# Optimization experiments

Measured on AMD Instinct MI355X. Metric: run time of the kernel, lower is better.

## Reference

```python
import jax, jax.numpy as jnp
import numpy as np

N = 30000        # nodes
E = 600000       # edges
R = 32           # relations
NB = 30          # num_bases
D = 128          # entity_dim == hidden_dim == output_dim
H = 8            # heads, head dim C = D // H = 16
NUM_ENT = 100000
NGRAPH = 16      # graphs in batch
L = 2            # num_rgcn_layers == num_transformer_layers
EPS = 1e-5


def _ln(x, g, b):
    mu = x.mean(-1, keepdims=True)
    var = ((x - mu) ** 2).mean(-1, keepdims=True)
    return (x - mu) * jax.lax.rsqrt(var + EPS) * g + b


def setup_inputs() -> dict:
    key = jax.random.key(0)
    ks = iter(jax.random.split(key, 48))

    def nrm(shape, s=0.05):
        return jax.random.normal(next(ks), shape, jnp.float32) * s

    inp = {}
    inp["node_ids"] = jax.random.randint(next(ks), (N,), 0, NUM_ENT)
    inp["edge_index"] = jax.random.randint(next(ks), (2, E), 0, N)
    inp["edge_type"] = jax.random.randint(next(ks), (E,), 0, R)
    inp["batch"] = jnp.sort(jax.random.randint(next(ks), (N,), 0, NGRAPH))
    inp["entity_emb"] = nrm((NUM_ENT, D)).at[0].set(0.0)  # padding_idx=0
    inp["rel_emb"] = nrm((R, D)).at[0].set(0.0)           # padding_idx=0
    inp["rgcn_comp"] = nrm((L, R, NB))
    inp["rgcn_bases"] = nrm((L, NB, D, D))
    inp["rgcn_root"] = nrm((L, D, D))
    inp["rgcn_bias"] = jnp.zeros((L, D), jnp.float32)
    inp["rgcn_ln_g"] = jnp.ones((L, D), jnp.float32)
    inp["rgcn_ln_b"] = jnp.zeros((L, D), jnp.float32)
    inp["tr_wq"] = nrm((L, D, D)); inp["tr_bq"] = jnp.zeros((L, D), jnp.float32)
    inp["tr_wk"] = nrm((L, D, D)); inp["tr_bk"] = jnp.zeros((L, D), jnp.float32)
    inp["tr_wv"] = nrm((L, D, D)); inp["tr_bv"] = jnp.zeros((L, D), jnp.float32)
    inp["tr_we"] = nrm((L, D, D))                          # lin_edge (bias=False in PyG)
    inp["tr_wskip"] = nrm((L, D, D)); inp["tr_bskip"] = jnp.zeros((L, D), jnp.float32)
    inp["tr_ln_g"] = jnp.ones((L, D), jnp.float32)
    inp["tr_ln_b"] = jnp.zeros((L, D), jnp.float32)
    return inp


def reference(node_ids, edge_index, edge_type, batch, entity_emb, rel_emb,
              rgcn_comp, rgcn_bases, rgcn_root, rgcn_bias, rgcn_ln_g, rgcn_ln_b,
              tr_wq, tr_bq, tr_wk, tr_bk, tr_wv, tr_bv, tr_we, tr_wskip, tr_bskip,
              tr_ln_g, tr_ln_b):
    src, tgt = edge_index[0], edge_index[1]
    C = D // H
    x = entity_emb[node_ids]            # [N, D]
    edge_attr = rel_emb[edge_type]      # [E, D]

    # ---- RGCN layers: basis decomposition, mean aggregation per (target, relation) ----
    seg = tgt * R + edge_type
    cnt = jax.ops.segment_sum(jnp.ones((E,), jnp.float32), seg, num_segments=N * R)
    inv = jnp.where(cnt > 0, 1.0 / jnp.maximum(cnt, 1.0), 0.0)   # [N*R]
    for l in range(L):
        agg = jax.ops.segment_sum(x[src], seg, num_segments=N * R)   # [N*R, D]
        agg = (agg * inv[:, None]).reshape(N, R, D)
        w = jnp.einsum('rb,bio->rio', rgcn_comp[l], rgcn_bases[l])   # [R, D, D]
        x = jnp.einsum('nri,rio->no', agg, w) + x @ rgcn_root[l] + rgcn_bias[l]
        x = jax.nn.relu(_ln(x, rgcn_ln_g[l], rgcn_ln_b[l]))          # dropout = identity (eval)

    # ---- TransformerConv layers: edge-conditioned multi-head attention ----
    for l in range(L):
        q = (x @ tr_wq[l] + tr_bq[l]).reshape(N, H, C)
        k = (x @ tr_wk[l] + tr_bk[l]).reshape(N, H, C)
        v = (x @ tr_wv[l] + tr_bv[l]).reshape(N, H, C)
        e = (edge_attr @ tr_we[l]).reshape(E, H, C)
        kj = k[src] + e                                              # [E, H, C]
        vj = v[src] + e
        alpha = jnp.einsum('ehc,ehc->eh', q[tgt], kj) / np.float32(np.sqrt(C))
        m = jax.ops.segment_max(alpha, tgt, num_segments=N)          # [N, H]
        a = jnp.exp(alpha - m[tgt])
        denom = jax.ops.segment_sum(a, tgt, num_segments=N)
        a = a / jnp.maximum(denom[tgt], 1e-16)                       # softmax per target node
        out = jax.ops.segment_sum((vj * a[:, :, None]).reshape(E, D), tgt, num_segments=N)
        out = out + x @ tr_wskip[l] + tr_bskip[l]                    # root/skip connection
        out = jax.nn.relu(_ln(out, tr_ln_g[l], tr_ln_b[l]))          # dropout = identity (eval)
        x = x + out                                                  # dims match -> residual

    cnt_g = jax.ops.segment_sum(jnp.ones((N,), jnp.float32), batch, num_segments=NGRAPH)
    graph_emb = jax.ops.segment_sum(x, batch, num_segments=NGRAPH) / jnp.maximum(cnt_g, 1.0)[:, None]
    return x, graph_emb
```

## Files before the change

kernel.cpp:

```cpp
#include <hip/hip_runtime.h>

#define NN 30000
#define NE 600000
#define RR 32
#define NBASE 30
#define NG 16

typedef long long i64;
typedef unsigned short ushort;
typedef short bf16x8 __attribute__((ext_vector_type(8)));
typedef float f32x4 __attribute__((ext_vector_type(4)));

__device__ __forceinline__ ushort f2bf(float f){
  unsigned u = __float_as_uint(f);
  u += 0x7fffu + ((u >> 16) & 1u);
  return (ushort)(u >> 16);
}
__device__ __forceinline__ float bf2f(ushort u){
  return __uint_as_float(((unsigned)u) << 16);
}
__device__ __forceinline__ unsigned pk2(float a, float b){
  return (unsigned)f2bf(a) | ((unsigned)f2bf(b) << 16);
}

__global__ void k_gather(const float* __restrict__ emb, const int* __restrict__ ids,
                         float* __restrict__ x, ushort* __restrict__ xb){
  int t = blockIdx.x*256 + threadIdx.x;
  if (t >= NN*32) return;
  int n = t >> 5, c = t & 31;
  float4 v = ((const float4*)emb)[(i64)ids[n]*32 + c];
  ((float4*)x)[(i64)n*32 + c] = v;
  *(uint2*)&xb[(i64)n*128 + c*4] = make_uint2(pk2(v.x, v.y), pk2(v.z, v.w));
}

__global__ __launch_bounds__(256) void k_stats(const int* __restrict__ etgt,
    const int* __restrict__ ety, float* __restrict__ cnt,
    int* __restrict__ hist, int* __restrict__ hist2){
  __shared__ int lh[RR];
  if (threadIdx.x < RR) lh[threadIdx.x] = 0;
  __syncthreads();
  int e0 = blockIdx.x*2048 + threadIdx.x;
  #pragma unroll
  for (int i = 0; i < 8; i++){
    int e = e0 + i*256;
    if (e < NE){
      int tgt = etgt[e], r = ety[e];
      atomicAdd(&lh[r], 1);
      atomicAdd(&hist2[tgt], 1);
      atomicAdd(&cnt[(i64)tgt*RR + r], 1.0f);
    }
  }
  __syncthreads();
  if (threadIdx.x < RR){
    int v = lh[threadIdx.x];
    if (v) atomicAdd(&hist[threadIdx.x], v);
  }
}

__global__ __launch_bounds__(1024) void k_scan2(const int* __restrict__ hist2,
    int* __restrict__ rowptr, int* __restrict__ cursor2,
    const int* __restrict__ hist, int* __restrict__ base,
    int* __restrict__ cursor, int* __restrict__ pb, int* __restrict__ pb64){
  int t = threadIdx.x;
  if (t == 0){
    int s = 0, p = 0, p64 = 0;
    for (int r = 0; r < RR; r++){
      base[r] = s; cursor[r] = s; pb[r] = p; pb64[r] = p64;
      s += hist[r]; p += (hist[r] + 127) >> 7; p64 += (hist[r] + 63) >> 6;
    }
    base[RR] = s; pb[RR] = p; pb64[RR] = p64;
  }
  __shared__ int s[1024];
  int bse = t*30;
  int loc[30];
  int sum = 0;
  #pragma unroll
  for (int i = 0; i < 30; i++){
    int v = (bse+i < NN) ? hist2[bse+i] : 0;
    loc[i] = sum; sum += v;
  }
  s[t] = sum; __syncthreads();
  for (int off = 1; off < 1024; off <<= 1){
    int v = (t >= off) ? s[t-off] : 0;
    __syncthreads();
    s[t] += v;
    __syncthreads();
  }
  int excl = (t > 0) ? s[t-1] : 0;
  #pragma unroll
  for (int i = 0; i < 30; i++){
    int idx = bse + i;
    if (idx <= NN){
      rowptr[idx] = excl + loc[i];
      if (idx < NN) cursor2[idx] = excl + loc[i];
    }
  }
}

__global__ void k_scatter2(const int* __restrict__ etgt, const int* __restrict__ esrc,
                           const int* __restrict__ ety, int* __restrict__ cursor2,
                           int2* __restrict__ se2, int* __restrict__ pos2){
  int e = blockIdx.x*256 + threadIdx.x;
  if (e >= NE) return;
  int q = atomicAdd(&cursor2[etgt[e]], 1);
  se2[q] = make_int2(esrc[e], ety[e]);
  pos2[e] = q;
  if (e < 8) se2[NE + e] = make_int2(0, 0);
}

__global__ __launch_bounds__(256) void k_scatter_blk(const int* __restrict__ ety,
    const int* __restrict__ esrc, const int* __restrict__ etgt,
    const int* __restrict__ pos2, const float* __restrict__ cnt,
    int* __restrict__ cursor, int* __restrict__ eord,
    int* __restrict__ sg_src, int* __restrict__ sg_p2, float* __restrict__ sg_inv){
  __shared__ int lh[RR];
  __shared__ int lb[RR];
  if (threadIdx.x < RR) lh[threadIdx.x] = 0;
  __syncthreads();
  int e0 = blockIdx.x*2048 + threadIdx.x;
  #pragma unroll
  for (int i = 0; i < 8; i++){
    int e = e0 + i*256;
    if (e < NE) atomicAdd(&lh[ety[e]], 1);
  }
  __syncthreads();
  if (threadIdx.x < RR){
    int c = lh[threadIdx.x];
    lb[threadIdx.x] = c ? atomicAdd(&cursor[threadIdx.x], c) : 0;
  }
  __syncthreads();
  if (threadIdx.x < RR) lh[threadIdx.x] = 0;
  __syncthreads();
  #pragma unroll
  for (int i = 0; i < 8; i++){
    int e = e0 + i*256;
    if (e < NE){
      int r = ety[e];
      int loc = atomicAdd(&lh[r], 1);
      int slot = lb[r] + loc;
      eord[slot]   = e;
      sg_src[slot] = esrc[e];
      sg_p2[slot]  = pos2[e];
      sg_inv[slot] = 1.0f / cnt[(i64)etgt[e]*RR + r];
    }
  }
}

__global__ void k_basis(const float* __restrict__ comp, const float* __restrict__ bases,
                        float* __restrict__ wT, ushort* __restrict__ wTb){
  int t = blockIdx.x*256 + threadIdx.x;
  int r = t >> 14, rem = t & 16383, c = rem >> 7, kk = rem & 127;
  float acc = 0.f;
  for (int b = 0; b < NBASE; b++)
    acc += comp[r*NBASE + b] * bases[(i64)b*16384 + kk*128 + c];
  wT[t] = acc;
  wTb[t] = f2bf(acc);
}

__global__ void k_tw(const float* __restrict__ root, const float* __restrict__ wq,
                     const float* __restrict__ wk, const float* __restrict__ wv,
                     const float* __restrict__ wsk, ushort* __restrict__ out){
  int z = blockIdx.y;
  const float* srcs[5] = {root, wq, wk, wv, wsk};
  const float* S = srcs[z >> 1] + (i64)(z & 1)*16384;
  int idx = blockIdx.x*256 + threadIdx.x;
  int c = idx >> 7, kk = idx & 127;
  out[(i64)z*16384 + idx] = f2bf(S[kk*128 + c]);
}


__global__ __launch_bounds__(256, 4) void k_mm_mfma(const ushort* __restrict__ xb,
    const ushort* __restrict__ wTb, const float* __restrict__ bias,
    float* __restrict__ Y, int nrows){
  __shared__ ushort Xs[16384];
  int t = threadIdx.x;
  int row0 = blockIdx.x * 128;
  for (int i = t; i < 2048; i += 256){
    int row = i >> 4, c = i & 15;
    int gr = min(row0 + row, nrows - 1);
    *(uint4*)((char*)Xs + row*256 + ((c*16) ^ ((row&7)<<4))) =
        *(const uint4*)((const char*)(xb + (i64)gr*128) + c*16);
  }
  __syncthreads();
  int w = t >> 6, l = t & 63;
  int wm = w >> 1, wn = w & 1;
  int lrow = l & 15, lg = l >> 4;
  int swz = (lrow & 7) << 4;
  const char* pX = (const char*)Xs + (wm*64 + lrow)*256;
  const char* pW = (const char*)wTb + (wn*64 + lrow)*256 + 16*lg;
  f32x4 acc[4][4] = {};
  #pragma unroll
  for (int ks = 0; ks < 4; ks++){
    int kb = (16*lg + 64*ks) ^ swz;
    bf16x8 a[4], bx[4];
    #pragma unroll
    for (int ns = 0; ns < 4; ns++) a[ns]  = *(const bf16x8*)(pW + ns*4096 + 64*ks);
    #pragma unroll
    for (int ms = 0; ms < 4; ms++) bx[ms] = *(const bf16x8*)(pX + ms*4096 + kb);
    #pragma unroll
    for (int ms = 0; ms < 4; ms++)
      #pragma unroll
      for (int ns = 0; ns < 4; ns++)
        acc[ms][ns] = __builtin_amdgcn_mfma_f32_16x16x32_bf16(a[ns], bx[ms], acc[ms][ns], 0, 0, 0);
  }
  #pragma unroll
  for (int ms = 0; ms < 4; ms++){
    int m = row0 + wm*64 + ms*16 + lrow;
    if (m >= nrows) continue;
    #pragma unroll
    for (int ns = 0; ns < 4; ns++){
      int n0 = wn*64 + ns*16 + 4*lg;
      float4 bv = *(const float4*)&bias[n0];
      f32x4 v = acc[ms][ns];
      *(float4*)&Y[(i64)m*128 + n0] =
          make_float4(v[0]+bv.x, v[1]+bv.y, v[2]+bv.z, v[3]+bv.w);
    }
  }
}

__global__ __launch_bounds__(256, 4) void k_mm4(const ushort* __restrict__ xb,
    const ushort* __restrict__ wTb, int layer,
    const float* __restrict__ biq, const float* __restrict__ bik,
    const float* __restrict__ biv, const float* __restrict__ bisk,
    ushort* __restrict__ qo, ushort* __restrict__ ko, ushort* __restrict__ vo,
    float* __restrict__ z, int nrows){
  __shared__ ushort Xs[16384];
  int t = threadIdx.x;
  int row0 = blockIdx.x * 128;
  for (int i = t; i < 2048; i += 256){
    int row = i >> 4, c = i & 15;
    int gr = min(row0 + row, nrows - 1);
    *(uint4*)((char*)Xs + row*256 + ((c*16) ^ ((row&7)<<4))) =
        *(const uint4*)((const char*)(xb + (i64)gr*128) + c*16);
  }
  __syncthreads();
  int w = t >> 6, l = t & 63;
  int wm = w >> 1, wn = w & 1;
  int lrow = l & 15, lg = l >> 4;
  int swz = (lrow & 7) << 4;
  const char* pX = (const char*)Xs + (wm*64 + lrow)*256;
  const float* biases[4] = {biq, bik, biv, bisk};
  ushort* outs[3] = {qo, ko, vo};
  #pragma unroll 1
  for (int arr = 0; arr < 4; arr++){
    const char* pW = (const char*)(wTb + (i64)(2 + 2*arr + layer)*16384)
                     + (wn*64 + lrow)*256 + 16*lg;
    f32x4 acc[4][4] = {};
    #pragma unroll
    for (int ks = 0; ks < 4; ks++){
      int kb = (16*lg + 64*ks) ^ swz;
      bf16x8 a[4], bx[4];
      #pragma unroll
      for (int ns = 0; ns < 4; ns++) a[ns]  = *(const bf16x8*)(pW + ns*4096 + 64*ks);
      #pragma unroll
      for (int ms = 0; ms < 4; ms++) bx[ms] = *(const bf16x8*)(pX + ms*4096 + kb);
      #pragma unroll
      for (int ms = 0; ms < 4; ms++)
        #pragma unroll
        for (int ns = 0; ns < 4; ns++)
          acc[ms][ns] = __builtin_amdgcn_mfma_f32_16x16x32_bf16(a[ns], bx[ms], acc[ms][ns], 0, 0, 0);
    }
    const float* bias = biases[arr];
    #pragma unroll
    for (int ms = 0; ms < 4; ms++){
      int m = row0 + wm*64 + ms*16 + lrow;
      if (m >= nrows) continue;
      #pragma unroll
      for (int ns = 0; ns < 4; ns++){
        int n0 = wn*64 + ns*16 + 4*lg;
        float4 bv = *(const float4*)&bias[n0];
        f32x4 v = acc[ms][ns];
        if (arr < 3){
          *(uint2*)&outs[arr][(i64)m*128 + n0] =
              make_uint2(pk2(v[0]+bv.x, v[1]+bv.y), pk2(v[2]+bv.z, v[3]+bv.w));
        } else {
          *(float4*)&z[(i64)m*128 + n0] =
              make_float4(v[0]+bv.x, v[1]+bv.y, v[2]+bv.z, v[3]+bv.w);
        }
      }
    }
  }
}

__global__ __launch_bounds__(256, 4) void k_edge_mfma(
    const int* __restrict__ sg_src, const int* __restrict__ sg_p2,
    const float* __restrict__ sg_inv, const int* __restrict__ hist,
    const int* __restrict__ base, const int* __restrict__ pb,
    const ushort* __restrict__ xb, const ushort* __restrict__ wb,
    ushort* __restrict__ y){
  __shared__ ushort Xs[16384];
  __shared__ int s_src[128];
  __shared__ int s_p2[128];
  __shared__ float s_inv[128];
  int b = blockIdx.x;
  int r = -1;
  #pragma unroll 1
  for (int i = 0; i < RR; i++){
    if (b >= pb[i] && b < pb[i+1]) { r = i; break; }
  }
  if (r < 0) return;
  int chunk = b - pb[r];
  int rowbase = base[r] + chunk*128;
  int nvalid = min(128, hist[r] - chunk*128);
  int t = threadIdx.x;
  if (t < 128){
    bool valid = t < nvalid;
    int slot = rowbase + (valid ? t : 0);
    s_src[t] = sg_src[slot];
    s_p2[t]  = valid ? sg_p2[slot] : NE;
    s_inv[t] = valid ? sg_inv[slot] : 0.0f;
  }
  __syncthreads();
  for (int i = t; i < 2048; i += 256){
    int row = i >> 4, c = i & 15;
    *(uint4*)((char*)Xs + row*256 + ((c*16) ^ ((row&7)<<4))) =
        *(const uint4*)((const char*)(xb + (i64)s_src[row]*128) + c*16);
  }
  __syncthreads();
  int w = t >> 6, l = t & 63;
  int wm = w >> 1, wn = w & 1;
  int lrow = l & 15, lg = l >> 4;
  int swz = (lrow & 7) << 4;
  const char* pX = (const char*)Xs + (wm*64 + lrow)*256;
  const char* pW = (const char*)(wb + (i64)r*16384) + (wn*64 + lrow)*256 + 16*lg;
  f32x4 acc[4][4] = {};
  #pragma unroll
  for (int ks = 0; ks < 4; ks++){
    int kb = (16*lg + 64*ks) ^ swz;
    bf16x8 a[4], bx[4];
    #pragma unroll
    for (int ns = 0; ns < 4; ns++) a[ns]  = *(const bf16x8*)(pW + ns*4096 + 64*ks);
    #pragma unroll
    for (int ms = 0; ms < 4; ms++) bx[ms] = *(const bf16x8*)(pX + ms*4096 + kb);
    #pragma unroll
    for (int ms = 0; ms < 4; ms++)
      #pragma unroll
      for (int ns = 0; ns < 4; ns++)
        acc[ms][ns] = __builtin_amdgcn_mfma_f32_16x16x32_bf16(a[ns], bx[ms], acc[ms][ns], 0, 0, 0);
  }
  __syncthreads();
  #pragma unroll
  for (int ms = 0; ms < 4; ms++){
    int m = wm*64 + ms*16 + lrow;
    float sc = s_inv[m];
    int msk = (m & 7) << 4;
    #pragma unroll
    for (int ns = 0; ns < 4; ns++){
      int n0 = wn*64 + ns*16 + 4*lg;
      f32x4 v = acc[ms][ns];
      *(uint2*)((char*)Xs + m*256 + ((n0*2) ^ msk)) =
          make_uint2(pk2(v[0]*sc, v[1]*sc), pk2(v[2]*sc, v[3]*sc));
    }
  }
  __syncthreads();
  for (int i = t; i < 2048; i += 256){
    int row = i >> 4, c = i & 15;
    uint4 v = *(const uint4*)((const char*)Xs + row*256 + ((c*16) ^ ((row&7)<<4)));
    *(uint4*)&y[(i64)s_p2[row]*128 + c*8] = v;
  }
}

__global__ __launch_bounds__(256) void k_edge_atomic(const int* __restrict__ esrc,
    const int* __restrict__ etgt, const int* __restrict__ eord,
    const int* __restrict__ hist, const int* __restrict__ base,
    const int* __restrict__ pb, const float* __restrict__ cnt,
    const float* __restrict__ x, const float* __restrict__ wT,
    float* __restrict__ z){
  __shared__ float Xs[64][132];
  __shared__ int s_src[64];
  __shared__ int s_tgt[64];
  __shared__ float s_inv[64];
  int b = blockIdx.x;
  int r = -1;
  #pragma unroll 1
  for (int i = 0; i < RR; i++){
    if (b >= pb[i] && b < pb[i+1]) { r = i; break; }
  }
  if (r < 0) return;
  int chunk = b - pb[r];
  int rowbase = base[r] + chunk*64;
  int cnt_r = hist[r];
  if (threadIdx.x < 64){
    int i = threadIdx.x;
    bool valid = (chunk*64 + i) < cnt_r;
    int eid = valid ? eord[rowbase + i] : 0;
    int sv = valid ? esrc[eid] : 0;
    int tv = valid ? etgt[eid] : 0;
    s_src[i] = sv; s_tgt[i] = tv;
    s_inv[i] = valid ? (1.0f / cnt[(i64)tv*RR + r]) : 0.0f;
  }
  __syncthreads();
  for (int idx = threadIdx.x; idx < 64*32; idx += 256){
    int rr = idx >> 5, c4 = idx & 31;
    *(float4*)&Xs[rr][c4*4] = ((const float4*)x)[(i64)s_src[rr]*32 + c4];
  }
  __syncthreads();
  const float* W = wT + (i64)r*16384;
  int m = threadIdx.x & 15, cg = threadIdx.x >> 4;
  float acc[4][8] = {};
  #pragma unroll 2
  for (int k4 = 0; k4 < 128; k4 += 4){
    float4 xv[4], wv[8];
    #pragma unroll
    for (int i = 0; i < 4; i++) xv[i] = *(float4*)&Xs[m + 16*i][k4];
    #pragma unroll
    for (int j = 0; j < 8; j++) wv[j] = *(const float4*)&W[(i64)(cg + 16*j)*128 + k4];
    #pragma unroll
    for (int i = 0; i < 4; i++)
      #pragma unroll
      for (int j = 0; j < 8; j++)
        acc[i][j] += xv[i].x*wv[j].x + xv[i].y*wv[j].y + xv[i].z*wv[j].z + xv[i].w*wv[j].w;
  }
  #pragma unroll
  for (int i = 0; i < 4; i++){
    int rr = m + 16*i;
    float sc = s_inv[rr];
    i64 o = (i64)s_tgt[rr]*128;
    #pragma unroll
    for (int j = 0; j < 8; j++)
      atomicAdd(&z[o + cg + 16*j], acc[i][j]*sc);
  }
}

__global__ void k_seg(const int* __restrict__ rowptr, const ushort* __restrict__ y,
                      const float* __restrict__ z, const float* __restrict__ g,
                      const float* __restrict__ b, float* __restrict__ x,
                      ushort* __restrict__ xb){
  int t = (blockIdx.x*256 + threadIdx.x) >> 6;
  int l = threadIdx.x & 63;
  if (t >= NN) return;
  int q0 = rowptr[t], q1 = rowptr[t+1];
  float ax = 0.f, ay = 0.f;
  for (int q = q0; q < q1; q++){
    ushort2 u = *(const ushort2*)&y[(i64)q*128 + 2*l];
    ax += bf2f(u.x); ay += bf2f(u.y);
  }
  float2 zv = *(const float2*)&z[(i64)t*128 + 2*l];
  float tx = ax + zv.x, ty = ay + zv.y;
  float s = tx + ty;
  #pragma unroll
  for (int o = 1; o < 64; o <<= 1) s += __shfl_xor(s, o);
  float mu = s * 0.0078125f;
  float dx = tx - mu, dy = ty - mu;
  float s2 = dx*dx + dy*dy;
  #pragma unroll
  for (int o = 1; o < 64; o <<= 1) s2 += __shfl_xor(s2, o);
  float rs = rsqrtf(s2 * 0.0078125f + 1e-5f);
  float2 gg = *(const float2*)&g[2*l];
  float2 bb = *(const float2*)&b[2*l];
  float o0 = fmaxf(dx*rs*gg.x + bb.x, 0.f);
  float o1 = fmaxf(dy*rs*gg.y + bb.y, 0.f);
  *(float2*)&x[(i64)t*128 + 2*l] = make_float2(o0, o1);
  *(unsigned*)&xb[(i64)t*128 + 2*l] = pk2(o0, o1);
}

__global__ void k_lnrelu(const float* __restrict__ z, const float* __restrict__ g,
                         const float* __restrict__ b, float* __restrict__ xo,
                         ushort* __restrict__ xb){
  int w = (blockIdx.x*256 + threadIdx.x) >> 6;
  int l = threadIdx.x & 63;
  if (w >= NN) return;
  float2 v = *(const float2*)&z[(i64)w*128 + 2*l];
  float s = v.x + v.y;
  #pragma unroll
  for (int o = 1; o < 64; o <<= 1) s += __shfl_xor(s, o);
  float mu = s * 0.0078125f;
  float dx = v.x - mu, dy = v.y - mu;
  float s2 = dx*dx + dy*dy;
  #pragma unroll
  for (int o = 1; o < 64; o <<= 1) s2 += __shfl_xor(s2, o);
  float rs = rsqrtf(s2 * 0.0078125f + 1e-5f);
  float2 gg = *(const float2*)&g[2*l];
  float2 bb = *(const float2*)&b[2*l];
  float o0 = fmaxf(dx*rs*gg.x + bb.x, 0.f);
  float o1 = fmaxf(dy*rs*gg.y + bb.y, 0.f);
  *(float2*)&xo[(i64)w*128 + 2*l] = make_float2(o0, o1);
  *(unsigned*)&xb[(i64)w*128 + 2*l] = pk2(o0, o1);
}

__global__ void k_ew(const float* __restrict__ rel, const float* __restrict__ we,
                     float* __restrict__ ew){
  int t = blockIdx.x*256 + threadIdx.x;
  int r = t >> 7, c = t & 127;
  float acc = 0.f;
  for (int k = 0; k < 128; k++) acc += rel[r*128 + k] * we[k*128 + c];
  ew[t] = acc;
}

__global__ __launch_bounds__(256) void k_attn(const int2* __restrict__ se2,
    const int* __restrict__ rowptr,
    const ushort* __restrict__ qbb, const ushort* __restrict__ kbb,
    const ushort* __restrict__ vbb, const float* __restrict__ ew,
    const float* __restrict__ sk, const float* __restrict__ g,
    const float* __restrict__ b, const float* __restrict__ xin,
    float* __restrict__ xout, ushort* __restrict__ xb){
  __shared__ float sew[RR*128];
  __shared__ float part[4][3][64];
  for (int i = threadIdx.x; i < RR*32; i += 256)
    ((float4*)sew)[i] = ((const float4*)ew)[i];
  __syncthreads();
  int wid = threadIdx.x >> 6;
  int half = wid & 1;
  int t = blockIdx.x*2 + (wid >> 1);
  int l = threadIdx.x & 63;
  int q0 = rowptr[t], q1 = rowptr[t+1];
  unsigned qu = *(const unsigned*)&qbb[(i64)t*128 + 2*l];
  float qx = bf2f((ushort)qu) * 0.25f, qy = bf2f((ushort)(qu >> 16)) * 0.25f;
  float den = 0.f, ox = 0.f, oy = 0.f;
  int qs = q0 + half;
  if (qs < q1){
    int2 s0 = se2[qs], s1 = se2[qs+2], s2 = se2[qs+4], s3 = se2[qs+6];
    unsigned ku0 = *(const unsigned*)&kbb[(i64)s0.x*128 + 2*l];
    unsigned vu0 = *(const unsigned*)&vbb[(i64)s0.x*128 + 2*l];
    unsigned ku1 = *(const unsigned*)&kbb[(i64)s1.x*128 + 2*l];
    unsigned vu1 = *(const unsigned*)&vbb[(i64)s1.x*128 + 2*l];
    unsigned ku2 = *(const unsigned*)&kbb[(i64)s2.x*128 + 2*l];
    unsigned vu2 = *(const unsigned*)&vbb[(i64)s2.x*128 + 2*l];
    unsigned ku3 = *(const unsigned*)&kbb[(i64)s3.x*128 + 2*l];
    unsigned vu3 = *(const unsigned*)&vbb[(i64)s3.x*128 + 2*l];
    for (int q = qs; q < q1; q += 2){
      int2 s4 = se2[q + 8];
      unsigned ku4 = *(const unsigned*)&kbb[(i64)s4.x*128 + 2*l];
      unsigned vu4 = *(const unsigned*)&vbb[(i64)s4.x*128 + 2*l];
      float2 ev = *(const float2*)&sew[s0.y*128 + 2*l];
      float kx = bf2f((ushort)ku0) + ev.x, ky = bf2f((ushort)(ku0 >> 16)) + ev.y;
      float p = qx*kx + qy*ky;
      p += __shfl_xor(p, 1); p += __shfl_xor(p, 2); p += __shfl_xor(p, 4);
      float wgt = __expf(p);
      den += wgt;
      ox += wgt*(bf2f((ushort)vu0) + ev.x);
      oy += wgt*(bf2f((ushort)(vu0 >> 16)) + ev.y);
      s0 = s1; s1 = s2; s2 = s3; s3 = s4;
      ku0 = ku1; ku1 = ku2; ku2 = ku3; ku3 = ku4;
      vu0 = vu1; vu1 = vu2; vu2 = vu3; vu3 = vu4;
    }
  }
  part[wid][0][l] = ox; part[wid][1][l] = oy; part[wid][2][l] = den;
  __syncthreads();
  if (half) return;
  ox  += part[wid^1][0][l];
  oy  += part[wid^1][1][l];
  den += part[wid^1][2][l];
  float dn = fmaxf(den, 1e-16f);
  float2 zv = *(const float2*)&sk[(i64)t*128 + 2*l];
  float tx = ox/dn + zv.x, ty = oy/dn + zv.y;
  float s = tx + ty;
  #pragma unroll
  for (int o = 1; o < 64; o <<= 1) s += __shfl_xor(s, o);
  float mu = s * 0.0078125f;
  float dx = tx - mu, dy = ty - mu;
  float s2 = dx*dx + dy*dy;
  #pragma unroll
  for (int o = 1; o < 64; o <<= 1) s2 += __shfl_xor(s2, o);
  float rs = rsqrtf(s2 * 0.0078125f + 1e-5f);
  float2 gg = *(const float2*)&g[2*l];
  float2 bb = *(const float2*)&b[2*l];
  float o0 = fmaxf(dx*rs*gg.x + bb.x, 0.f);
  float o1 = fmaxf(dy*rs*gg.y + bb.y, 0.f);
  float2 xv = *(const float2*)&xin[(i64)t*128 + 2*l];
  float nx = xv.x + o0, ny = xv.y + o1;
  *(float2*)&xout[(i64)t*128 + 2*l] = make_float2(nx, ny);
  *(unsigned*)&xb[(i64)t*128 + 2*l] = pk2(nx, ny);
}

__global__ void k_cntg(const int* __restrict__ batch, float* __restrict__ cntg){
  __shared__ int lh[NG];
  if (threadIdx.x < NG) lh[threadIdx.x] = 0;
  __syncthreads();
  int n = blockIdx.x*256 + threadIdx.x;
  if (n < NN) atomicAdd(&lh[batch[n]], 1);
  __syncthreads();
  if (threadIdx.x < NG){
    int v = lh[threadIdx.x];
    if (v) atomicAdd(&cntg[threadIdx.x], (float)v);
  }
}

__global__ void k_pool(const float* __restrict__ x, const int* __restrict__ batch,
                       float* __restrict__ gsum){
  __shared__ float acc[NG*128];
  for (int i = threadIdx.x; i < NG*128; i += 256) acc[i] = 0.f;
  __syncthreads();
  int per = (NN + gridDim.x - 1) / gridDim.x;
  int n0 = blockIdx.x*per, n1 = min(n0 + per, NN);
  int sub = threadIdx.x >> 5, c4 = threadIdx.x & 31;
  for (int n = n0 + sub; n < n1; n += 8){
    int g = batch[n];
    float4 xv = ((const float4*)x)[(i64)n*32 + c4];
    atomicAdd(&acc[g*128 + c4*4 + 0], xv.x);
    atomicAdd(&acc[g*128 + c4*4 + 1], xv.y);
    atomicAdd(&acc[g*128 + c4*4 + 2], xv.z);
    atomicAdd(&acc[g*128 + c4*4 + 3], xv.w);
  }
  __syncthreads();
  for (int i = threadIdx.x; i < NG*128; i += 256) atomicAdd(&gsum[i], acc[i]);
}

__global__ void k_poolfin(const float* __restrict__ gsum, const float* __restrict__ cntg,
                          float* __restrict__ gout){
  int t = blockIdx.x*256 + threadIdx.x;
  int g = t >> 7;
  gout[t] = gsum[t] / fmaxf(cntg[g], 1.0f);
}

extern "C" void kernel_launch(void* const* d_in, const int* in_sizes, int n_in,
                              void* d_out, int out_size, void* d_ws, size_t ws_size,
                              hipStream_t stream) {
  const int*   node_ids = (const int*)d_in[0];
  const int*   eidx  = (const int*)d_in[1];
  const int*   esrc  = eidx;
  const int*   etgt  = eidx + NE;
  const int*   ety   = (const int*)d_in[2];
  const int*   batch = (const int*)d_in[3];
  const float* ent   = (const float*)d_in[4];
  const float* rel   = (const float*)d_in[5];
  const float* comp  = (const float*)d_in[6];
  const float* bases = (const float*)d_in[7];
  const float* root  = (const float*)d_in[8];
  const float* rbias = (const float*)d_in[9];
  const float* rlng  = (const float*)d_in[10];
  const float* rlnb  = (const float*)d_in[11];
  const float* wq    = (const float*)d_in[12];
  const float* bq    = (const float*)d_in[13];
  const float* wk    = (const float*)d_in[14];
  const float* bk    = (const float*)d_in[15];
  const float* wv    = (const float*)d_in[16];
  const float* bv    = (const float*)d_in[17];
  const float* we    = (const float*)d_in[18];
  const float* wsk   = (const float*)d_in[19];
  const float* bsk   = (const float*)d_in[20];
  const float* tlng  = (const float*)d_in[21];
  const float* tlnb  = (const float*)d_in[22];
  float* out = (float*)d_out;

  char* wp = (char*)d_ws;
  auto alloc = [&](size_t bytes)->void*{
    void* p = (void*)wp;
    wp += (bytes + 255) & ~(size_t)255;
    return p;
  };
  float*    x     = (float*)alloc((size_t)NN*128*4);
  ushort*   xb    = (ushort*)alloc((size_t)NN*128*2);
  float*    z     = (float*)alloc((size_t)NN*128*4);
  ushort*   qbb   = (ushort*)alloc((size_t)NN*128*2);
  ushort*   kbb   = (ushort*)alloc((size_t)NN*128*2);
  ushort*   vbb   = (ushort*)alloc((size_t)NN*128*2);
  float*    cnt   = (float*)alloc((size_t)NN*RR*4);
  float*    wbT   = (float*)alloc((size_t)RR*16384*4);
  ushort*   wbTb  = (ushort*)alloc((size_t)RR*16384*2);
  ushort*   wTb   = (ushort*)alloc((size_t)10*16384*2);
  float*    ew    = (float*)alloc((size_t)RR*128*4);
  int*      eord  = (int*)alloc((size_t)NE*4);
  int*      pos2  = (int*)alloc((size_t)NE*4);
  int2*     se2   = (int2*)alloc((size_t)(NE + 8)*8);
  int*      sg_src= (int*)alloc((size_t)NE*4);
  int*      sg_p2 = (int*)alloc((size_t)NE*4);
  float*    sg_inv= (float*)alloc((size_t)NE*4);
  int*      hist  = (int*)alloc(RR*4);
  int*      base  = (int*)alloc((RR+1)*4);
  int*      cursor= (int*)alloc(RR*4);
  int*      pb    = (int*)alloc((RR+1)*4);
  int*      pb64  = (int*)alloc((RR+1)*4);
  int*      hist2 = (int*)alloc((size_t)NN*4);
  int*      rowptr= (int*)alloc((size_t)(NN+1)*4);
  int*      cursor2=(int*)alloc((size_t)NN*4);
  float*    cntg  = (float*)alloc(NG*4);
  float*    gsum  = (float*)alloc((size_t)NG*128*4);
  size_t ybytes = (size_t)(NE + 8)*128*2;
  ushort*   y     = (ushort*)alloc(ybytes);
  bool fast = ((char*)y + ybytes) <= ((char*)d_ws + ws_size);

  dim3 B(256);

  hipMemsetAsync(cnt, 0, (size_t)NN*RR*4, stream);
  hipMemsetAsync(hist, 0, RR*4, stream);
  hipMemsetAsync(hist2, 0, (size_t)NN*4, stream);

  k_gather<<<3750, B, 0, stream>>>(ent, node_ids, x, xb);
  k_stats<<<294, B, 0, stream>>>(etgt, ety, cnt, hist, hist2);
  k_scan2<<<1, 1024, 0, stream>>>(hist2, rowptr, cursor2, hist, base, cursor, pb, pb64);
  k_scatter2<<<2344, B, 0, stream>>>(etgt, esrc, ety, cursor2, se2, pos2);
  k_scatter_blk<<<294, B, 0, stream>>>(ety, esrc, etgt, pos2, cnt, cursor, eord,
                                       sg_src, sg_p2, sg_inv);
  k_tw<<<dim3(64,10), B, 0, stream>>>(root, wq, wk, wv, wsk, wTb);

  for (int l = 0; l < 2; l++){
    k_basis<<<2048, B, 0, stream>>>(comp + l*RR*NBASE, bases + (i64)l*NBASE*16384, wbT, wbTb);
    k_mm_mfma<<<235, B, 0, stream>>>(xb, wTb + (i64)(0 + l)*16384, rbias + l*128, z, NN);
    if (fast){
      k_edge_mfma<<<4720, B, 0, stream>>>(sg_src, sg_p2, sg_inv, hist, base, pb, xb, wbTb, y);
      k_seg<<<7500, B, 0, stream>>>(rowptr, y, z, rlng + l*128, rlnb + l*128, x, xb);
    } else {
      k_edge_atomic<<<9407, B, 0, stream>>>(esrc, etgt, eord, hist, base, pb64, cnt, x, wbT, z);
      k_lnrelu<<<7500, B, 0, stream>>>(z, rlng + l*128, rlnb + l*128, x, xb);
    }
  }

  for (int l = 0; l < 2; l++){
    k_ew<<<16, B, 0, stream>>>(rel, we + (i64)l*16384, ew);
    k_mm4<<<235, B, 0, stream>>>(xb, wTb, l, bq + l*128, bk + l*128, bv + l*128,
                                 bsk + l*128, qbb, kbb, vbb, z, NN);
    k_attn<<<15000, B, 0, stream>>>(se2, rowptr, qbb, kbb, vbb, ew, z,
                                    tlng + l*128, tlnb + l*128, x,
                                    (l == 1) ? out : x, xb);
  }

  hipMemsetAsync(gsum, 0, (size_t)NG*128*4, stream);
  hipMemsetAsync(cntg, 0, NG*4, stream);
  k_cntg<<<118, B, 0, stream>>>(batch, cntg);
  k_pool<<<120, B, 0, stream>>>(out, batch, gsum);
  k_poolfin<<<8, B, 0, stream>>>(gsum, cntg, out + (i64)NN*128);
}
```

Baseline: 865.5 us.

## Batch per-layer weight precompute, fuse graph counts into gather, simplify attention

The basis-weight and edge-projection kernels now run once for both layers instead of once per layer, and the per-graph node count is folded into the gather kernel, which removes several launches. Attention goes from two waves per node (interleaved edges merged through shared memory) to one wave per node with a 4-deep prefetch, dropping the extra synchronisation and shared merge but halving the parallelism per node. The RGCN segment sum is unrolled by two. Costs include larger workspace buffers for the weights of both layers and longer serial edge loops per wave in attention.

```diff
diff --git a/kernel.cpp b/kernel.cpp
--- a/kernel.cpp
+++ b/kernel.cpp
@@ -23,14 +23,23 @@
   return (unsigned)f2bf(a) | ((unsigned)f2bf(b) << 16);
 }
 
-__global__ void k_gather(const float* __restrict__ emb, const int* __restrict__ ids,
-                         float* __restrict__ x, ushort* __restrict__ xb){
+__global__ __launch_bounds__(256) void k_gather(const float* __restrict__ emb,
+    const int* __restrict__ ids, const int* __restrict__ batch,
+    float* __restrict__ x, ushort* __restrict__ xb, float* __restrict__ cntg){
+  __shared__ int lh[NG];
+  if (threadIdx.x < NG) lh[threadIdx.x] = 0;
+  __syncthreads();
   int t = blockIdx.x*256 + threadIdx.x;
-  if (t >= NN*32) return;
   int n = t >> 5, c = t & 31;
   float4 v = ((const float4*)emb)[(i64)ids[n]*32 + c];
   ((float4*)x)[(i64)n*32 + c] = v;
   *(uint2*)&xb[(i64)n*128 + c*4] = make_uint2(pk2(v.x, v.y), pk2(v.z, v.w));
+  if (c == 0) atomicAdd(&lh[batch[n]], 1);
+  __syncthreads();
+  if (threadIdx.x < NG){
+    int cv = lh[threadIdx.x];
+    if (cv) atomicAdd(&cntg[threadIdx.x], (float)cv);
+  }
 }
 
 __global__ __launch_bounds__(256) void k_stats(const int* __restrict__ etgt,
@@ -149,10 +158,14 @@
 __global__ void k_basis(const float* __restrict__ comp, const float* __restrict__ bases,
                         float* __restrict__ wT, ushort* __restrict__ wTb){
   int t = blockIdx.x*256 + threadIdx.x;
-  int r = t >> 14, rem = t & 16383, c = rem >> 7, kk = rem & 127;
+  int lyr = t >> 19;
+  int rem = t & 524287;
+  int r = rem >> 14, rem2 = rem & 16383, c = rem2 >> 7, kk = rem2 & 127;
+  const float* cp = comp + (i64)lyr*RR*NBASE + r*NBASE;
+  const float* bs = bases + (i64)lyr*NBASE*16384;
   float acc = 0.f;
   for (int b = 0; b < NBASE; b++)
-    acc += comp[r*NBASE + b] * bases[(i64)b*16384 + kk*128 + c];
+    acc += cp[b] * bs[(i64)b*16384 + kk*128 + c];
   wT[t] = acc;
   wTb[t] = f2bf(acc);
 }
@@ -166,6 +179,18 @@
   int idx = blockIdx.x*256 + threadIdx.x;
   int c = idx >> 7, kk = idx & 127;
   out[(i64)z*16384 + idx] = f2bf(S[kk*128 + c]);
+}
+
+__global__ void k_ew(const float* __restrict__ rel, const float* __restrict__ we,
+                     float* __restrict__ ew){
+  int t = blockIdx.x*256 + threadIdx.x;
+  int lr = t >> 12;
+  int rem = t & 4095;
+  int r = rem >> 7, c = rem & 127;
+  const float* W = we + (i64)lr*16384;
+  float acc = 0.f;
+  for (int k = 0; k < 128; k++) acc += rel[r*128 + k] * W[k*128 + c];
+  ew[t] = acc;
 }
 
 
@@ -431,7 +456,14 @@
   if (t >= NN) return;
   int q0 = rowptr[t], q1 = rowptr[t+1];
   float ax = 0.f, ay = 0.f;
-  for (int q = q0; q < q1; q++){
+  int q = q0;
+  for (; q + 1 < q1; q += 2){
+    ushort2 u0 = *(const ushort2*)&y[(i64)q*128 + 2*l];
+    ushort2 u1 = *(const ushort2*)&y[(i64)(q+1)*128 + 2*l];
+    ax += bf2f(u0.x) + bf2f(u1.x);
+    ay += bf2f(u0.y) + bf2f(u1.y);
+  }
+  if (q < q1){
     ushort2 u = *(const ushort2*)&y[(i64)q*128 + 2*l];
     ax += bf2f(u.x); ay += bf2f(u.y);
   }
@@ -478,15 +510,6 @@
   *(unsigned*)&xb[(i64)w*128 + 2*l] = pk2(o0, o1);
 }
 
-__global__ void k_ew(const float* __restrict__ rel, const float* __restrict__ we,
-                     float* __restrict__ ew){
-  int t = blockIdx.x*256 + threadIdx.x;
-  int r = t >> 7, c = t & 127;
-  float acc = 0.f;
-  for (int k = 0; k < 128; k++) acc += rel[r*128 + k] * we[k*128 + c];
-  ew[t] = acc;
-}
-
 __global__ __launch_bounds__(256) void k_attn(const int2* __restrict__ se2,
     const int* __restrict__ rowptr,
     const ushort* __restrict__ qbb, const ushort* __restrict__ kbb,
@@ -495,21 +518,18 @@
     const float* __restrict__ b, const float* __restrict__ xin,
     float* __restrict__ xout, ushort* __restrict__ xb){
   __shared__ float sew[RR*128];
-  __shared__ float part[4][3][64];
   for (int i = threadIdx.x; i < RR*32; i += 256)
     ((float4*)sew)[i] = ((const float4*)ew)[i];
   __syncthreads();
   int wid = threadIdx.x >> 6;
-  int half = wid & 1;
-  int t = blockIdx.x*2 + (wid >> 1);
+  int t = blockIdx.x*4 + wid;
   int l = threadIdx.x & 63;
   int q0 = rowptr[t], q1 = rowptr[t+1];
   unsigned qu = *(const unsigned*)&qbb[(i64)t*128 + 2*l];
   float qx = bf2f((ushort)qu) * 0.25f, qy = bf2f((ushort)(qu >> 16)) * 0.25f;
   float den = 0.f, ox = 0.f, oy = 0.f;
-  int qs = q0 + half;
-  if (qs < q1){
-    int2 s0 = se2[qs], s1 = se2[qs+2], s2 = se2[qs+4], s3 = se2[qs+6];
+  if (q0 < q1){
+    int2 s0 = se2[q0], s1 = se2[q0+1], s2 = se2[q0+2], s3 = se2[q0+3];
     unsigned ku0 = *(const unsigned*)&kbb[(i64)s0.x*128 + 2*l];
     unsigned vu0 = *(const unsigned*)&vbb[(i64)s0.x*128 + 2*l];
     unsigned ku1 = *(const unsigned*)&kbb[(i64)s1.x*128 + 2*l];
@@ -518,8 +538,8 @@
     unsigned vu2 = *(const unsigned*)&vbb[(i64)s2.x*128 + 2*l];
     unsigned ku3 = *(const unsigned*)&kbb[(i64)s3.x*128 + 2*l];
     unsigned vu3 = *(const unsigned*)&vbb[(i64)s3.x*128 + 2*l];
-    for (int q = qs; q < q1; q += 2){
-      int2 s4 = se2[q + 8];
+    for (int q = q0; q < q1; q++){
+      int2 s4 = se2[q + 4];
       unsigned ku4 = *(const unsigned*)&kbb[(i64)s4.x*128 + 2*l];
       unsigned vu4 = *(const unsigned*)&vbb[(i64)s4.x*128 + 2*l];
       float2 ev = *(const float2*)&sew[s0.y*128 + 2*l];
@@ -535,12 +555,6 @@
       vu0 = vu1; vu1 = vu2; vu2 = vu3; vu3 = vu4;
     }
   }
-  part[wid][0][l] = ox; part[wid][1][l] = oy; part[wid][2][l] = den;
-  __syncthreads();
-  if (half) return;
-  ox  += part[wid^1][0][l];
-  oy  += part[wid^1][1][l];
-  den += part[wid^1][2][l];
   float dn = fmaxf(den, 1e-16f);
   float2 zv = *(const float2*)&sk[(i64)t*128 + 2*l];
   float tx = ox/dn + zv.x, ty = oy/dn + zv.y;
@@ -561,19 +575,6 @@
   float nx = xv.x + o0, ny = xv.y + o1;
   *(float2*)&xout[(i64)t*128 + 2*l] = make_float2(nx, ny);
   *(unsigned*)&xb[(i64)t*128 + 2*l] = pk2(nx, ny);
-}
-
-__global__ void k_cntg(const int* __restrict__ batch, float* __restrict__ cntg){
-  __shared__ int lh[NG];
-  if (threadIdx.x < NG) lh[threadIdx.x] = 0;
-  __syncthreads();
-  int n = blockIdx.x*256 + threadIdx.x;
-  if (n < NN) atomicAdd(&lh[batch[n]], 1);
-  __syncthreads();
-  if (threadIdx.x < NG){
-    int v = lh[threadIdx.x];
-    if (v) atomicAdd(&cntg[threadIdx.x], (float)v);
-  }
 }
 
 __global__ void k_pool(const float* __restrict__ x, const int* __restrict__ batch,
@@ -646,10 +647,10 @@
   ushort*   kbb   = (ushort*)alloc((size_t)NN*128*2);
   ushort*   vbb   = (ushort*)alloc((size_t)NN*128*2);
   float*    cnt   = (float*)alloc((size_t)NN*RR*4);
-  float*    wbT   = (float*)alloc((size_t)RR*16384*4);
-  ushort*   wbTb  = (ushort*)alloc((size_t)RR*16384*2);
+  float*    wbT   = (float*)alloc((size_t)2*RR*16384*4);
+  ushort*   wbTb  = (ushort*)alloc((size_t)2*RR*16384*2);
   ushort*   wTb   = (ushort*)alloc((size_t)10*16384*2);
-  float*    ew    = (float*)alloc((size_t)RR*128*4);
+  float*    ew    = (float*)alloc((size_t)2*RR*128*4);
   int*      eord  = (int*)alloc((size_t)NE*4);
   int*      pos2  = (int*)alloc((size_t)NE*4);
   int2*     se2   = (int2*)alloc((size_t)(NE + 8)*8);
@@ -675,39 +676,40 @@
   hipMemsetAsync(cnt, 0, (size_t)NN*RR*4, stream);
   hipMemsetAsync(hist, 0, RR*4, stream);
   hipMemsetAsync(hist2, 0, (size_t)NN*4, stream);
-
-  k_gather<<<3750, B, 0, stream>>>(ent, node_ids, x, xb);
+  hipMemsetAsync(cntg, 0, NG*4, stream);
+
+  k_gather<<<3750, B, 0, stream>>>(ent, node_ids, batch, x, xb, cntg);
   k_stats<<<294, B, 0, stream>>>(etgt, ety, cnt, hist, hist2);
   k_scan2<<<1, 1024, 0, stream>>>(hist2, rowptr, cursor2, hist, base, cursor, pb, pb64);
   k_scatter2<<<2344, B, 0, stream>>>(etgt, esrc, ety, cursor2, se2, pos2);
   k_scatter_blk<<<294, B, 0, stream>>>(ety, esrc, etgt, pos2, cnt, cursor, eord,
                                        sg_src, sg_p2, sg_inv);
   k_tw<<<dim3(64,10), B, 0, stream>>>(root, wq, wk, wv, wsk, wTb);
+  k_basis<<<4096, B, 0, stream>>>(comp, bases, wbT, wbTb);
+  k_ew<<<32, B, 0, stream>>>(rel, we, ew);
 
   for (int l = 0; l < 2; l++){
-    k_basis<<<2048, B, 0, stream>>>(comp + l*RR*NBASE, bases + (i64)l*NBASE*16384, wbT, wbTb);
     k_mm_mfma<<<235, B, 0, stream>>>(xb, wTb + (i64)(0 + l)*16384, rbias + l*128, z, NN);
     if (fast){
-      k_edge_mfma<<<4720, B, 0, stream>>>(sg_src, sg_p2, sg_inv, hist, base, pb, xb, wbTb, y);
+      k_edge_mfma<<<4720, B, 0, stream>>>(sg_src, sg_p2, sg_inv, hist, base, pb,
+                                          xb, wbTb + (i64)l*RR*16384, y);
       k_seg<<<7500, B, 0, stream>>>(rowptr, y, z, rlng + l*128, rlnb + l*128, x, xb);
     } else {
-      k_edge_atomic<<<9407, B, 0, stream>>>(esrc, etgt, eord, hist, base, pb64, cnt, x, wbT, z);
+      k_edge_atomic<<<9407, B, 0, stream>>>(esrc, etgt, eord, hist, base, pb64, cnt,
+                                            x, wbT + (i64)l*RR*16384, z);
       k_lnrelu<<<7500, B, 0, stream>>>(z, rlng + l*128, rlnb + l*128, x, xb);
     }
   }
 
   for (int l = 0; l < 2; l++){
-    k_ew<<<16, B, 0, stream>>>(rel, we + (i64)l*16384, ew);
     k_mm4<<<235, B, 0, stream>>>(xb, wTb, l, bq + l*128, bk + l*128, bv + l*128,
                                  bsk + l*128, qbb, kbb, vbb, z, NN);
-    k_attn<<<15000, B, 0, stream>>>(se2, rowptr, qbb, kbb, vbb, ew, z,
-                                    tlng + l*128, tlnb + l*128, x,
-                                    (l == 1) ? out : x, xb);
+    k_attn<<<7500, B, 0, stream>>>(se2, rowptr, qbb, kbb, vbb, ew + (i64)l*RR*128, z,
+                                   tlng + l*128, tlnb + l*128, x,
+                                   (l == 1) ? out : x, xb);
   }
 
   hipMemsetAsync(gsum, 0, (size_t)NG*128*4, stream);
-  hipMemsetAsync(cntg, 0, NG*4, stream);
-  k_cntg<<<118, B, 0, stream>>>(batch, cntg);
   k_pool<<<120, B, 0, stream>>>(out, batch, gsum);
   k_poolfin<<<8, B, 0, stream>>>(gsum, cntg, out + (i64)NN*128);
 }
```

After: 875.3 us. No clear change (+1.1%).
